# Kernel tuning notes

Measured on AMD Instinct MI355X. Metric: run time of the kernel, lower is better.

## Reference

```python
import jax, jax.numpy as jnp
import numpy as np

T, D, F_, E, K = 8192, 1024, 4096, 8, 2


def setup_inputs() -> dict:
    key = jax.random.key(0)
    ks = jax.random.split(key, 5)
    s_d = 1.0 / np.sqrt(D)
    s_f = 1.0 / np.sqrt(F_)
    return {
        "x": jax.random.normal(ks[0], (T, D), dtype=jnp.float32),
        "gate_w": jax.random.normal(ks[1], (D, E), dtype=jnp.float32) * s_d,
        "w1": jax.random.normal(ks[2], (E, D, F_), dtype=jnp.float32) * s_d,  # up (gate proj)
        "w3": jax.random.normal(ks[3], (E, D, F_), dtype=jnp.float32) * s_d,  # up (value proj)
        "w2": jax.random.normal(ks[4], (E, F_, D), dtype=jnp.float32) * s_f,  # down proj
    }


def reference(x, gate_w, w1, w2, w3):
    # gate + top-k routing
    logits = x @ gate_w                                   # [T, E]
    top_w, top_idx = jax.lax.top_k(logits, K)             # [T, K]
    w = jax.nn.softmax(top_w.astype(jnp.float32), axis=-1).astype(x.dtype)
    # combine[t, e] = routing weight of token t for expert e (0 if unrouted)
    combine = jnp.sum(w[:, :, None] * jax.nn.one_hot(top_idx, E, dtype=x.dtype), axis=1)  # [T, E]
    # dense dispatch: each expert processes all tokens, masked by combine weight
    # (identical math to the torch gather/scatter loop: unrouted tokens get weight 0)
    out = jnp.zeros_like(x)
    for e in range(E):
        h = jax.nn.silu(x @ w1[e]) * (x @ w3[e])          # [T, F] SwiGLU
        out = out + combine[:, e:e + 1] * (h @ w2[e])     # [T, D]
    return out
```

## Files before the change

kernel.cpp:

```cpp
#include <hip/hip_runtime.h>
#include <stdint.h>

#define T_TOK 8192
#define D_DIM 1024
#define F_DIM 4096
#define E_NUM 8
#define RCAP  17408
#define MT    136

typedef __bf16 bf16;
typedef __bf16 bf16x8 __attribute__((ext_vector_type(8)));
typedef float  f32x4  __attribute__((ext_vector_type(4)));

typedef const __attribute__((address_space(1))) void* gptr1;
typedef __attribute__((address_space(3))) void* lptr3;

__device__ __forceinline__ void gload_lds16(const void* g, void* l) {
    __builtin_amdgcn_global_load_lds((gptr1)g, (lptr3)l, 16, 0, 0);
}

__device__ __forceinline__ unsigned short f2b(float f) {
    uint32_t u = __float_as_uint(f);
    u = (u + 0x7FFFu + ((u >> 16) & 1u)) >> 16;
    return (unsigned short)u;
}

__global__ __launch_bounds__(256) void trans_kernel(const float* __restrict__ src,
                                                    bf16* __restrict__ dst,
                                                    int R, int C) {
    __shared__ unsigned short lt[64 * 72];
    const int e  = blockIdx.z;
    const int c0 = blockIdx.x * 64;
    const int r0 = blockIdx.y * 64;
    const float* s = src + (size_t)e * R * C;
    unsigned short* dp = (unsigned short*)dst + (size_t)e * R * C;
    const int t  = threadIdx.x;
    const int tr = t >> 4;
    const int tc = (t & 15) * 4;
    #pragma unroll
    for (int rr = 0; rr < 4; ++rr) {
        const int r = tr + rr * 16;
        const float4 v = *(const float4*)(s + (size_t)(r0 + r) * C + c0 + tc);
        lt[(tc + 0) * 72 + r] = f2b(v.x);
        lt[(tc + 1) * 72 + r] = f2b(v.y);
        lt[(tc + 2) * 72 + r] = f2b(v.z);
        lt[(tc + 3) * 72 + r] = f2b(v.w);
    }
    __syncthreads();
    const int oc  = t >> 2;
    const int seg = (t & 3) * 16;
    const uint4 a = *(const uint4*)&lt[oc * 72 + seg];
    const uint4 b = *(const uint4*)&lt[oc * 72 + seg + 8];
    unsigned short* orow = dp + (size_t)(c0 + oc) * R + (r0 + seg);
    *(uint4*)(orow)     = a;
    *(uint4*)(orow + 8) = b;
}

__global__ __launch_bounds__(256) void gate_kernel(const float* __restrict__ x,
                                                   const float* __restrict__ gw,
                                                   int* __restrict__ tki,
                                                   float* __restrict__ tkw,
                                                   int* __restrict__ counts) {
    const int t    = blockIdx.x * 4 + (threadIdx.x >> 6);
    const int lane = threadIdx.x & 63;
    const float* xr = x + (size_t)t * D_DIM;
    float acc[E_NUM];
    #pragma unroll
    for (int e = 0; e < E_NUM; ++e) acc[e] = 0.f;
    for (int j = 0; j < 16; ++j) {
        const int d = lane + 64 * j;
        const float xv = xr[d];
        const float* g = gw + (size_t)d * E_NUM;
        #pragma unroll
        for (int e = 0; e < E_NUM; ++e) acc[e] += xv * g[e];
    }
    #pragma unroll
    for (int off = 32; off >= 1; off >>= 1) {
        #pragma unroll
        for (int e = 0; e < E_NUM; ++e) acc[e] += __shfl_xor(acc[e], off);
    }
    if (lane == 0) {
        int b0 = 0; float v0 = acc[0];
        #pragma unroll
        for (int e = 1; e < E_NUM; ++e) if (acc[e] > v0) { v0 = acc[e]; b0 = e; }
        int b1 = -1; float v1 = -1e30f;
        #pragma unroll
        for (int e = 0; e < E_NUM; ++e) if (e != b0 && acc[e] > v1) { v1 = acc[e]; b1 = e; }
        const float ex = expf(v1 - v0);
        const float w0 = 1.f / (1.f + ex);
        const float w1 = ex * w0;
        tki[t * 2]     = b0;  tkw[t * 2]     = w0;
        tki[t * 2 + 1] = b1;  tkw[t * 2 + 1] = w1;
        atomicAdd(&counts[b0], 1);
        atomicAdd(&counts[b1], 1);
    }
}

__global__ void scan_kernel(const int* __restrict__ counts, int* __restrict__ aoff,
                            int* __restrict__ cursor) {
    if (threadIdx.x == 0) {
        int off = 0;
        #pragma unroll
        for (int e = 0; e < E_NUM; ++e) {
            aoff[e]   = off;
            cursor[e] = off;
            off += (counts[e] + 127) & ~127;
        }
        aoff[E_NUM] = off;
    }
}

__global__ __launch_bounds__(256) void gather_kernel(const float* __restrict__ x,
                                                     const int* __restrict__ tki,
                                                     const float* __restrict__ tkw,
                                                     int* __restrict__ cursor,
                                                     int* __restrict__ ptok,
                                                     float* __restrict__ pwgt,
                                                     bf16* __restrict__ xp) {
    const int slot = blockIdx.x * 4 + (threadIdx.x >> 6);
    const int lane = threadIdx.x & 63;
    const int t = slot >> 1;
    int row = 0;
    if (lane == 0) {
        const int e = tki[slot];
        row = atomicAdd(&cursor[e], 1);
        ptok[row] = t;
        pwgt[row] = tkw[slot];
    }
    row = __shfl(row, 0);
    const float* xr = x + (size_t)t * D_DIM + lane * 16;
    unsigned short* dst = (unsigned short*)xp + (size_t)row * D_DIM + lane * 16;
    uint32_t u[8];
    #pragma unroll
    for (int q = 0; q < 4; ++q) {
        const float4 v = *(const float4*)(xr + q * 4);
        u[q * 2]     = (uint32_t)f2b(v.x) | ((uint32_t)f2b(v.y) << 16);
        u[q * 2 + 1] = (uint32_t)f2b(v.z) | ((uint32_t)f2b(v.w) << 16);
    }
    ((uint4*)dst)[0] = make_uint4(u[0], u[1], u[2], u[3]);
    ((uint4*)dst)[1] = make_uint4(u[4], u[5], u[6], u[7]);
}

__global__ __launch_bounds__(256, 2) void gemm1_kernel(const bf16* __restrict__ xp,
                                                       const bf16* __restrict__ wb1t,
                                                       const bf16* __restrict__ wb3t,
                                                       bf16* __restrict__ hb,
                                                       const int* __restrict__ aoff,
                                                       const int* __restrict__ counts) {
    __shared__ bf16 As[128 * 32];
    __shared__ bf16 Bs1[128 * 32];
    __shared__ bf16 Bs3[128 * 32];

    const int m_base = blockIdx.y * 128;
    int e = 0;
    #pragma unroll
    for (int i = 1; i < E_NUM; ++i) if (m_base >= aoff[i]) e = i;
    if (m_base - aoff[e] >= counts[e]) return;

    const int nt   = blockIdx.x;
    const int tid  = threadIdx.x;
    const int w    = tid >> 6;
    const int lane = tid & 63;
    const int wm   = w & 1, wn = w >> 1;

    const bf16* Ab = xp + (size_t)m_base * D_DIM;
    const bf16* B1 = wb1t + ((size_t)e * F_DIM + (size_t)nt * 128) * D_DIM;
    const bf16* B3 = wb3t + ((size_t)e * F_DIM + (size_t)nt * 128) * D_DIM;

    const int srow    = w * 32 + (lane >> 2);
    const int scol    = (lane & 3) * 8;
    const int ldsbase = w * 1024;
    const int fm = lane & 15;
    const int fk = (lane >> 4) * 8;

    f32x4 acc1[4][4] = {};
    f32x4 acc3[4][4] = {};

    for (int kt = 0; kt < D_DIM / 32; ++kt) {
        const int k0 = kt * 32;
        #pragma unroll
        for (int j = 0; j < 2; ++j) {
            const size_t go = (size_t)(srow + j * 16) * D_DIM + (k0 + scol);
            gload_lds16(Ab + go, &As[ldsbase + j * 512]);
            gload_lds16(B1 + go, &Bs1[ldsbase + j * 512]);
            gload_lds16(B3 + go, &Bs3[ldsbase + j * 512]);
        }
        __syncthreads();
        bf16x8 af[4], b1f[4], b3f[4];
        #pragma unroll
        for (int i = 0; i < 4; ++i) {
            af[i]  = *(const bf16x8*)&As [(wm * 64 + i * 16 + fm) * 32 + fk];
            b1f[i] = *(const bf16x8*)&Bs1[(wn * 64 + i * 16 + fm) * 32 + fk];
            b3f[i] = *(const bf16x8*)&Bs3[(wn * 64 + i * 16 + fm) * 32 + fk];
        }
        #pragma unroll
        for (int i = 0; i < 4; ++i) {
            #pragma unroll
            for (int jn = 0; jn < 4; ++jn) {
                acc1[i][jn] = __builtin_amdgcn_mfma_f32_16x16x32_bf16(af[i], b1f[jn], acc1[i][jn], 0, 0, 0);
                acc3[i][jn] = __builtin_amdgcn_mfma_f32_16x16x32_bf16(af[i], b3f[jn], acc3[i][jn], 0, 0, 0);
            }
        }
        __syncthreads();
    }

    unsigned short* hw = (unsigned short*)hb;
    #pragma unroll
    for (int i = 0; i < 4; ++i) {
        const int rbase = m_base + wm * 64 + i * 16 + (lane >> 4) * 4;
        #pragma unroll
        for (int jn = 0; jn < 4; ++jn) {
            const int col = nt * 128 + wn * 64 + jn * 16 + (lane & 15);
            #pragma unroll
            for (int r = 0; r < 4; ++r) {
                const float s1 = acc1[i][jn][r];
                const float s3 = acc3[i][jn][r];
                const float hv = (s1 / (1.0f + __expf(-s1))) * s3;
                hw[(size_t)(rbase + r) * F_DIM + col] = f2b(hv);
            }
        }
    }
}

__global__ __launch_bounds__(256, 2) void gemm2_kernel(const bf16* __restrict__ hb,
                                                       const bf16* __restrict__ wb2t,
                                                       float* __restrict__ out,
                                                       const int* __restrict__ aoff,
                                                       const int* __restrict__ counts,
                                                       const int* __restrict__ ptok,
                                                       const float* __restrict__ pwgt) {
    __shared__ bf16 As[128 * 32];
    __shared__ bf16 Bs[128 * 32];

    const int m_base = blockIdx.y * 128;
    int e = 0;
    #pragma unroll
    for (int i = 1; i < E_NUM; ++i) if (m_base >= aoff[i]) e = i;
    if (m_base - aoff[e] >= counts[e]) return;

    const int nt   = blockIdx.x;
    const int tid  = threadIdx.x;
    const int w    = tid >> 6;
    const int lane = tid & 63;
    const int wm   = w & 1, wn = w >> 1;

    const bf16* Ab = hb + (size_t)m_base * F_DIM;
    const bf16* Bb = wb2t + ((size_t)e * D_DIM + (size_t)nt * 128) * F_DIM;

    const int srow    = w * 32 + (lane >> 2);
    const int scol    = (lane & 3) * 8;
    const int ldsbase = w * 1024;
    const int fm = lane & 15;
    const int fk = (lane >> 4) * 8;

    f32x4 acc[4][4] = {};

    for (int kt = 0; kt < F_DIM / 32; ++kt) {
        const int k0 = kt * 32;
        #pragma unroll
        for (int j = 0; j < 2; ++j) {
            const size_t go = (size_t)(srow + j * 16) * F_DIM + (k0 + scol);
            gload_lds16(Ab + go, &As[ldsbase + j * 512]);
            gload_lds16(Bb + go, &Bs[ldsbase + j * 512]);
        }
        __syncthreads();
        bf16x8 af[4], bfr[4];
        #pragma unroll
        for (int i = 0; i < 4; ++i) {
            af[i]  = *(const bf16x8*)&As[(wm * 64 + i * 16 + fm) * 32 + fk];
            bfr[i] = *(const bf16x8*)&Bs[(wn * 64 + i * 16 + fm) * 32 + fk];
        }
        #pragma unroll
        for (int i = 0; i < 4; ++i) {
            #pragma unroll
            for (int jn = 0; jn < 4; ++jn) {
                acc[i][jn] = __builtin_amdgcn_mfma_f32_16x16x32_bf16(af[i], bfr[jn], acc[i][jn], 0, 0, 0);
            }
        }
        __syncthreads();
    }

    #pragma unroll
    for (int i = 0; i < 4; ++i) {
        const int rb = m_base + wm * 64 + i * 16 + (lane >> 4) * 4;
        #pragma unroll
        for (int r = 0; r < 4; ++r) {
            const int row = rb + r;
            const int tok = ptok[row];
            if (tok < 0) continue;
            const float wgt = pwgt[row];
            float* orow = out + (size_t)tok * D_DIM;
            #pragma unroll
            for (int jn = 0; jn < 4; ++jn) {
                const int col = nt * 128 + wn * 64 + jn * 16 + (lane & 15);
                atomicAdd(&orow[col], acc[i][jn][r] * wgt);
            }
        }
    }
}

extern "C" void kernel_launch(void* const* d_in, const int* in_sizes, int n_in,
                              void* d_out, int out_size, void* d_ws, size_t ws_size,
                              hipStream_t stream) {
    const float* x  = (const float*)d_in[0];
    const float* gw = (const float*)d_in[1];
    const float* w1 = (const float*)d_in[2];
    const float* w3 = (const float*)d_in[3];
    const float* w2 = (const float*)d_in[4];
    float* out = (float*)d_out;

    char* ws = (char*)d_ws;
    size_t off = 0;
    bf16* wb1t = (bf16*)(ws + off);
    bf16* wb2t = wb1t;
    off += (size_t)E_NUM * F_DIM * D_DIM * 2;
    bf16* wb3t = (bf16*)(ws + off); off += (size_t)E_NUM * F_DIM * D_DIM * 2;
    bf16* xp   = (bf16*)(ws + off); off += (size_t)RCAP * D_DIM * 2;
    bf16* hb   = (bf16*)(ws + off); off += (size_t)RCAP * F_DIM * 2;
    int*   tki = (int*)(ws + off);   off += (size_t)T_TOK * 2 * 4;
    float* tkw = (float*)(ws + off); off += (size_t)T_TOK * 2 * 4;
    int* counts = (int*)(ws + off);  off += 64;
    int* cursor = (int*)(ws + off);  off += 64;
    int* aoff   = (int*)(ws + off);  off += 64;
    int* ptok   = (int*)(ws + off);  off += (size_t)RCAP * 4;
    float* pwgt = (float*)(ws + off); off += (size_t)RCAP * 4;

    hipMemsetAsync(out, 0, (size_t)T_TOK * D_DIM * 4, stream);
    hipMemsetAsync(counts, 0, 64, stream);
    hipMemsetAsync(ptok, 0xFF, (size_t)RCAP * 4, stream);

    gate_kernel<<<T_TOK / 4, 256, 0, stream>>>(x, gw, tki, tkw, counts);
    scan_kernel<<<1, 64, 0, stream>>>(counts, aoff, cursor);
    gather_kernel<<<(T_TOK * 2) / 4, 256, 0, stream>>>(x, tki, tkw, cursor, ptok, pwgt, xp);

    trans_kernel<<<dim3(F_DIM / 64, D_DIM / 64, E_NUM), 256, 0, stream>>>(w1, wb1t, D_DIM, F_DIM);
    trans_kernel<<<dim3(F_DIM / 64, D_DIM / 64, E_NUM), 256, 0, stream>>>(w3, wb3t, D_DIM, F_DIM);

    gemm1_kernel<<<dim3(F_DIM / 128, MT), 256, 0, stream>>>(xp, wb1t, wb3t, hb, aoff, counts);

    trans_kernel<<<dim3(D_DIM / 64, F_DIM / 64, E_NUM), 256, 0, stream>>>(w2, wb2t, F_DIM, D_DIM);

    gemm2_kernel<<<dim3(D_DIM / 128, MT), 256, 0, stream>>>(hb, wb2t, out, aoff, counts, ptok, pwgt);
}
```

Before: 1.441 ms.

## Replace atomic scatter with per-row expert outputs and combine kernel; swizzle LDS

The down-projection GEMM now writes each permuted row's fp32 result into a scratch buffer, reusing the freed w3 transpose storage, instead of atomically adding weighted rows into the output. A new combine kernel gathers each token's two expert rows by slot index and blends them with the routing weights. This removes the output memset, the ptok memset and contended float atomics, at the cost of an extra fp32 round trip through memory. Separately, both GEMMs XOR-swizzle the LDS column layout to reduce bank conflicts on fragment reads.

```diff
diff --git a/kernel.cpp b/kernel.cpp
--- a/kernel.cpp
+++ b/kernel.cpp
@@ -112,10 +112,8 @@
 
 __global__ __launch_bounds__(256) void gather_kernel(const float* __restrict__ x,
                                                      const int* __restrict__ tki,
-                                                     const float* __restrict__ tkw,
                                                      int* __restrict__ cursor,
-                                                     int* __restrict__ ptok,
-                                                     float* __restrict__ pwgt,
+                                                     int* __restrict__ s2r,
                                                      bf16* __restrict__ xp) {
     const int slot = blockIdx.x * 4 + (threadIdx.x >> 6);
     const int lane = threadIdx.x & 63;
@@ -124,8 +122,7 @@
     if (lane == 0) {
         const int e = tki[slot];
         row = atomicAdd(&cursor[e], 1);
-        ptok[row] = t;
-        pwgt[row] = tkw[slot];
+        s2r[slot] = row;
     }
     row = __shfl(row, 0);
     const float* xr = x + (size_t)t * D_DIM + lane * 16;
@@ -167,11 +164,13 @@
     const bf16* B1 = wb1t + ((size_t)e * F_DIM + (size_t)nt * 128) * D_DIM;
     const bf16* B3 = wb3t + ((size_t)e * F_DIM + (size_t)nt * 128) * D_DIM;
 
-    const int srow    = w * 32 + (lane >> 2);
-    const int scol    = (lane & 3) * 8;
+    const int lr16 = lane >> 2;
+    const int cg   = lane & 3;
+    const int srow = w * 32 + lr16;
+    const int scol = (cg ^ ((lr16 >> 1) & 3)) * 8;
     const int ldsbase = w * 1024;
     const int fm = lane & 15;
-    const int fk = (lane >> 4) * 8;
+    const int fk = (((lane >> 4) ^ ((fm >> 1) & 3))) * 8;
 
     f32x4 acc1[4][4] = {};
     f32x4 acc3[4][4] = {};
@@ -224,11 +223,9 @@
 
 __global__ __launch_bounds__(256, 2) void gemm2_kernel(const bf16* __restrict__ hb,
                                                        const bf16* __restrict__ wb2t,
-                                                       float* __restrict__ out,
+                                                       float* __restrict__ yb,
                                                        const int* __restrict__ aoff,
-                                                       const int* __restrict__ counts,
-                                                       const int* __restrict__ ptok,
-                                                       const float* __restrict__ pwgt) {
+                                                       const int* __restrict__ counts) {
     __shared__ bf16 As[128 * 32];
     __shared__ bf16 Bs[128 * 32];
 
@@ -247,11 +244,13 @@
     const bf16* Ab = hb + (size_t)m_base * F_DIM;
     const bf16* Bb = wb2t + ((size_t)e * D_DIM + (size_t)nt * 128) * F_DIM;
 
-    const int srow    = w * 32 + (lane >> 2);
-    const int scol    = (lane & 3) * 8;
+    const int lr16 = lane >> 2;
+    const int cg   = lane & 3;
+    const int srow = w * 32 + lr16;
+    const int scol = (cg ^ ((lr16 >> 1) & 3)) * 8;
     const int ldsbase = w * 1024;
     const int fm = lane & 15;
-    const int fk = (lane >> 4) * 8;
+    const int fk = (((lane >> 4) ^ ((fm >> 1) & 3))) * 8;
 
     f32x4 acc[4][4] = {};
 
@@ -285,18 +284,33 @@
         const int rb = m_base + wm * 64 + i * 16 + (lane >> 4) * 4;
         #pragma unroll
         for (int r = 0; r < 4; ++r) {
-            const int row = rb + r;
-            const int tok = ptok[row];
-            if (tok < 0) continue;
-            const float wgt = pwgt[row];
-            float* orow = out + (size_t)tok * D_DIM;
+            float* yrow = yb + (size_t)(rb + r) * D_DIM;
             #pragma unroll
             for (int jn = 0; jn < 4; ++jn) {
                 const int col = nt * 128 + wn * 64 + jn * 16 + (lane & 15);
-                atomicAdd(&orow[col], acc[i][jn][r] * wgt);
+                yrow[col] = acc[i][jn][r];
             }
         }
     }
+}
+
+__global__ __launch_bounds__(256) void combine_kernel(const float* __restrict__ yb,
+                                                      const int* __restrict__ s2r,
+                                                      const float* __restrict__ tkw,
+                                                      float* __restrict__ out) {
+    const int idx = blockIdx.x * 256 + threadIdx.x;
+    const int t = idx >> 8;
+    const int c = (idx & 255) * 4;
+    const int r0 = s2r[t * 2], r1 = s2r[t * 2 + 1];
+    const float w0 = tkw[t * 2], w1 = tkw[t * 2 + 1];
+    const float4 a = *(const float4*)(yb + (size_t)r0 * D_DIM + c);
+    const float4 b = *(const float4*)(yb + (size_t)r1 * D_DIM + c);
+    float4 o;
+    o.x = w0 * a.x + w1 * b.x;
+    o.y = w0 * a.y + w1 * b.y;
+    o.z = w0 * a.z + w1 * b.z;
+    o.w = w0 * a.w + w1 * b.w;
+    *(float4*)(out + (size_t)t * D_DIM + c) = o;
 }
 
 extern "C" void kernel_launch(void* const* d_in, const int* in_sizes, int n_in,
@@ -314,7 +328,9 @@
     bf16* wb1t = (bf16*)(ws + off);
     bf16* wb2t = wb1t;
     off += (size_t)E_NUM * F_DIM * D_DIM * 2;
-    bf16* wb3t = (bf16*)(ws + off); off += (size_t)E_NUM * F_DIM * D_DIM * 2;
+    bf16* wb3t = (bf16*)(ws + off);
+    float* yb  = (float*)wb3t;
+    off += (size_t)E_NUM * F_DIM * D_DIM * 2;
     bf16* xp   = (bf16*)(ws + off); off += (size_t)RCAP * D_DIM * 2;
     bf16* hb   = (bf16*)(ws + off); off += (size_t)RCAP * F_DIM * 2;
     int*   tki = (int*)(ws + off);   off += (size_t)T_TOK * 2 * 4;
@@ -322,16 +338,13 @@
     int* counts = (int*)(ws + off);  off += 64;
     int* cursor = (int*)(ws + off);  off += 64;
     int* aoff   = (int*)(ws + off);  off += 64;
-    int* ptok   = (int*)(ws + off);  off += (size_t)RCAP * 4;
-    float* pwgt = (float*)(ws + off); off += (size_t)RCAP * 4;
-
-    hipMemsetAsync(out, 0, (size_t)T_TOK * D_DIM * 4, stream);
+    int* s2r    = (int*)(ws + off);  off += (size_t)T_TOK * 2 * 4;
+
     hipMemsetAsync(counts, 0, 64, stream);
-    hipMemsetAsync(ptok, 0xFF, (size_t)RCAP * 4, stream);
 
     gate_kernel<<<T_TOK / 4, 256, 0, stream>>>(x, gw, tki, tkw, counts);
     scan_kernel<<<1, 64, 0, stream>>>(counts, aoff, cursor);
-    gather_kernel<<<(T_TOK * 2) / 4, 256, 0, stream>>>(x, tki, tkw, cursor, ptok, pwgt, xp);
+    gather_kernel<<<(T_TOK * 2) / 4, 256, 0, stream>>>(x, tki, cursor, s2r, xp);
 
     trans_kernel<<<dim3(F_DIM / 64, D_DIM / 64, E_NUM), 256, 0, stream>>>(w1, wb1t, D_DIM, F_DIM);
     trans_kernel<<<dim3(F_DIM / 64, D_DIM / 64, E_NUM), 256, 0, stream>>>(w3, wb3t, D_DIM, F_DIM);
@@ -340,5 +353,7 @@
 
     trans_kernel<<<dim3(D_DIM / 64, F_DIM / 64, E_NUM), 256, 0, stream>>>(w2, wb2t, F_DIM, D_DIM);
 
-    gemm2_kernel<<<dim3(D_DIM / 128, MT), 256, 0, stream>>>(hb, wb2t, out, aoff, counts, ptok, pwgt);
-}
+    gemm2_kernel<<<dim3(D_DIM / 128, MT), 256, 0, stream>>>(hb, wb2t, yb, aoff, counts);
+
+    combine_kernel<<<(T_TOK * 256) / 256, 256, 0, stream>>>(yb, s2r, tkw, out);
+}
```

Result: faster. 1.402 ms (-2.7%).
